# Optimization experiments

Measured on AMD Instinct MI355X. Metric: run time of the kernel, lower is better.

Reference implementation:

```python
import jax, jax.numpy as jnp
import numpy as np

N_NODES = 100000
N_EDGES = 600000
D_FEAT = 128
N_CLASSES = 40
K = 2


def setup_inputs() -> dict:
    key = jax.random.key(0)
    k1, k2, k3, k4, k5 = jax.random.split(key, 5)
    x = jax.random.normal(k1, (N_NODES, D_FEAT), dtype=jnp.float32)
    edge_index = jax.random.randint(k2, (2, N_EDGES), 0, N_NODES, dtype=jnp.int64)
    W = jax.random.normal(k3, (N_CLASSES, D_FEAT), dtype=jnp.float32) / np.sqrt(D_FEAT)
    b = jax.random.normal(k4, (N_CLASSES,), dtype=jnp.float32) * 0.01
    return {"x": x, "edge_index": edge_index, "W": W, "b": b}


def _gcn_norm(edge_index, num_nodes):
    # add self loops (PyG gcn_norm default), edge_weight = 1
    loop = jnp.arange(num_nodes, dtype=edge_index.dtype)
    src = jnp.concatenate([edge_index[0], loop])
    dst = jnp.concatenate([edge_index[1], loop])
    w = jnp.ones(src.shape[0], dtype=jnp.float32)
    deg = jax.ops.segment_sum(w, dst, num_segments=num_nodes)  # [N]
    dinv = jnp.where(deg > 0, 1.0 / jnp.sqrt(deg), 0.0)
    norm = dinv[src] * w * dinv[dst]  # D^-1/2 A_hat D^-1/2 edge weights
    return src, dst, norm


def reference(x, edge_index, W, b):
    # eval mode: dropout is identity
    src, dst, norm = _gcn_norm(edge_index, N_NODES)
    for _ in range(K):
        # message: x_j * norm, aggr='add' at target nodes
        x = jax.ops.segment_sum(x[src] * norm[:, None], dst, num_segments=N_NODES)
    logits = x @ W.T + b  # [N, C]
    return jax.nn.log_softmax(logits, axis=1)
```

## Files before the change

### kernel.cpp

```cpp
#include <hip/hip_runtime.h>

#define N_NODES   100000
#define N_EDGES   600000
#define D_FEAT    128
#define N_CLASSES 40
#define USTRIDE   64
#define MAXW      40

#define NPAD      100352
#define N_TILES   (N_NODES / 16)
#define G_GEMM    1568
#define EPB       384
#define G_ZERO    (NPAD / 4 / 256 + 1)

typedef __attribute__((ext_vector_type(8))) short bf16x8;
typedef __attribute__((ext_vector_type(4))) float f32x4;

__device__ __forceinline__ float bf2f(unsigned int h) { return __uint_as_float(h << 16); }
__device__ __forceinline__ unsigned int f2bf(float f) {
    unsigned int u = __float_as_uint(f);
    return (u + 0x7FFFu + ((u >> 16) & 1u)) >> 16;
}
__device__ __forceinline__ float4 up4(uint2 v) {
    return make_float4(bf2f(v.x & 0xFFFFu), bf2f(v.x >> 16),
                       bf2f(v.y & 0xFFFFu), bf2f(v.y >> 16));
}
__device__ __forceinline__ uint2 pk4(float4 f) {
    uint2 r;
    r.x = f2bf(f.x) | (f2bf(f.y) << 16);
    r.y = f2bf(f.z) | (f2bf(f.w) << 16);
    return r;
}


__global__ void k_zero_wconv(int4* __restrict__ deg4, const float* __restrict__ W,
                             uint4* __restrict__ wfrag) {
    int t = threadIdx.x;
    if (blockIdx.x < G_ZERO - 1) {
        int i = blockIdx.x * 256 + t;
        if (i < NPAD / 4) deg4[i] = make_int4(0, 0, 0, 0);
        return;
    }
    for (int idx = t; idx < 768; idx += 256) {
        int lane = idx & 63;
        int kc   = (idx >> 6) & 3;
        int ct   = idx >> 8;
        int r16  = lane & 15;
        int g    = lane >> 4;
        int j    = ct * 16 + r16;
        uint4 o = make_uint4(0u, 0u, 0u, 0u);
        if (j < N_CLASSES) {
            const float* wr = W + (size_t)j * D_FEAT + kc * 32 + g * 8;
            float4 w0 = *(const float4*)wr;
            float4 w1 = *(const float4*)(wr + 4);
            o.x = f2bf(w0.x) | (f2bf(w0.y) << 16);
            o.y = f2bf(w0.z) | (f2bf(w0.w) << 16);
            o.z = f2bf(w1.x) | (f2bf(w1.y) << 16);
            o.w = f2bf(w1.z) | (f2bf(w1.w) << 16);
        }
        wfrag[idx] = o;
    }
}


__global__ __launch_bounds__(256) void k_gemm_ell(const float* __restrict__ x,
                                                  const uint4* __restrict__ wfrag,
                                                  unsigned short* __restrict__ y0,
                                                  const int* __restrict__ esrc,
                                                  const int* __restrict__ edst,
                                                  int* __restrict__ deg,
                                                  int* __restrict__ ell) {
    int t = threadIdx.x;
    int wid = t >> 6;
    int lane = t & 63;
    int tile = (blockIdx.x & 7) + 8 * ((blockIdx.x >> 3) * 4 + wid);
    bool valid = tile < N_TILES;

    int r16 = lane & 15;
    int g   = lane >> 4;
    int node = tile * 16 + r16;

    int e0 = blockIdx.x * EPB + t;
    int e1 = e0 + 256;
    bool v0 = e0 < N_EDGES;
    bool v1 = (t < EPB - 256) && (e1 < N_EDGES);
    int d0 = 0, d1 = 0, src0 = 0, src1 = 0;
    if (v0) { d0 = edst[e0]; src0 = esrc[e0]; }
    if (v1) { d1 = edst[e1]; src1 = esrc[e1]; }

    uint4 wq[12];
    float4 xv[8];
    if (valid) {
#pragma unroll
        for (int f = 0; f < 12; ++f) wq[f] = wfrag[f * 64 + lane];
        const float4* xp = (const float4*)(x + (size_t)node * D_FEAT);
#pragma unroll
        for (int kc = 0; kc < 4; ++kc) {
            xv[kc * 2]     = xp[kc * 8 + g * 2];
            xv[kc * 2 + 1] = xp[kc * 8 + g * 2 + 1];
        }
    }

    int o0 = 0, o1 = 0;
    if (v0) o0 = atomicAdd(&deg[d0], 1);
    if (v1) o1 = atomicAdd(&deg[d1], 1);

    bf16x8 afrag[4];
    if (valid) {
#pragma unroll
        for (int kc = 0; kc < 4; ++kc) {
            union { bf16x8 v; unsigned int u[4]; } a;
            a.u[0] = f2bf(xv[kc * 2].x) | (f2bf(xv[kc * 2].y) << 16);
            a.u[1] = f2bf(xv[kc * 2].z) | (f2bf(xv[kc * 2].w) << 16);
            a.u[2] = f2bf(xv[kc * 2 + 1].x) | (f2bf(xv[kc * 2 + 1].y) << 16);
            a.u[3] = f2bf(xv[kc * 2 + 1].z) | (f2bf(xv[kc * 2 + 1].w) << 16);
            afrag[kc] = a.v;
        }
    }

    f32x4 z = {0.f, 0.f, 0.f, 0.f};
    f32x4 acc0 = z, acc1 = z, acc2 = z;
    if (valid) {
#pragma unroll
        for (int kc = 0; kc < 4; ++kc) {
            union { uint4 u4; bf16x8 v; } b0, b1, b2;
            b0.u4 = wq[kc];  b1.u4 = wq[4 + kc];  b2.u4 = wq[8 + kc];
            acc0 = __builtin_amdgcn_mfma_f32_16x16x32_bf16(b0.v, afrag[kc], acc0, 0, 0, 0);
            acc1 = __builtin_amdgcn_mfma_f32_16x16x32_bf16(b1.v, afrag[kc], acc1, 0, 0, 0);
            acc2 = __builtin_amdgcn_mfma_f32_16x16x32_bf16(b2.v, afrag[kc], acc2, 0, 0, 0);
        }
    }

    if (v0 && o0 < MAXW) ell[(size_t)o0 * N_NODES + d0] = src0;
    if (v1 && o1 < MAXW) ell[(size_t)o1 * N_NODES + d1] = src1;

    if (!valid) return;

    unsigned short* orow = y0 + (size_t)node * USTRIDE;
    uint2 s0, s1;
    s0.x = f2bf(acc0[0]) | (f2bf(acc0[1]) << 16);
    s0.y = f2bf(acc0[2]) | (f2bf(acc0[3]) << 16);
    *(uint2*)(orow + g * 4) = s0;
    s1.x = f2bf(acc1[0]) | (f2bf(acc1[1]) << 16);
    s1.y = f2bf(acc1[2]) | (f2bf(acc1[3]) << 16);
    *(uint2*)(orow + 16 + g * 4) = s1;
    if (g < 2) {
        uint2 s2;
        s2.x = f2bf(acc2[0]) | (f2bf(acc2[1]) << 16);
        s2.y = f2bf(acc2[2]) | (f2bf(acc2[3]) << 16);
        *(uint2*)(orow + 32 + g * 4) = s2;
    } else {
        *(uint4*)(orow + 32 + g * 8) = make_uint4(0u, 0u, 0u, 0u);
    }
    if (g == 1) *(uint4*)(orow + 40) = make_uint4(0u, 0u, 0u, 0u);
}


__global__ __launch_bounds__(256) void k_gather1(const unsigned short* __restrict__ y0,
                                                 unsigned short* __restrict__ u1,
                                                 const int* __restrict__ deg,
                                                 const int* __restrict__ ell) {
    int t = blockIdx.x * blockDim.x + threadIdx.x;
    int i = t >> 4;
    if (i >= N_NODES) return;
    int sub = t & 1;
    int par = (t >> 1) & 7;
    const uint2* yb = (const uint2*)y0;

    int degi = deg[i];
    float di = rsqrtf((float)(degi + 1));

    float4 a[5];
    if (par == 0) {
        const uint2* self = yb + (size_t)i * 16 + sub * 5;
#pragma unroll
        for (int r = 0; r < 5; ++r) {
            float4 v = up4(self[r]);
            a[r] = make_float4(v.x * di, v.y * di, v.z * di, v.w * di);
        }
    } else {
#pragma unroll
        for (int r = 0; r < 5; ++r) a[r] = make_float4(0.f, 0.f, 0.f, 0.f);
    }

    int nd = degi < MAXW ? degi : MAXW;
    for (int k = par; k < nd; k += 8) {
        int s = ell[(size_t)k * N_NODES + i];
        float ds = rsqrtf((float)(deg[s] + 1));
        const uint2* p = yb + (size_t)s * 16 + sub * 5;
        uint2 w[5];
#pragma unroll
        for (int r = 0; r < 5; ++r) w[r] = p[r];
#pragma unroll
        for (int r = 0; r < 5; ++r) {
            float4 v = up4(w[r]);
            a[r].x += v.x * ds; a[r].y += v.y * ds;
            a[r].z += v.z * ds; a[r].w += v.w * ds;
        }
    }

#pragma unroll
    for (int d = 2; d <= 8; d <<= 1) {
#pragma unroll
        for (int r = 0; r < 5; ++r) {
            a[r].x += __shfl_xor(a[r].x, d); a[r].y += __shfl_xor(a[r].y, d);
            a[r].z += __shfl_xor(a[r].z, d); a[r].w += __shfl_xor(a[r].w, d);
        }
    }

    unsigned short* orow = u1 + (size_t)i * USTRIDE;
    if (par == 0) {
        float s2 = di * di;
        uint2* o = (uint2*)orow + sub * 5;
#pragma unroll
        for (int r = 0; r < 5; ++r) {
            o[r] = pk4(make_float4(a[r].x * s2, a[r].y * s2, a[r].z * s2, a[r].w * s2));
        }
    } else if (par == 1) {
        *(uint4*)(orow + 40 + sub * 8) = make_uint4(0u, 0u, 0u, 0u);
    } else if (par == 2 && sub == 0) {
        *(uint4*)(orow + 56) = make_uint4(0u, 0u, 0u, 0u);
    }
}


__global__ __launch_bounds__(256) void k_gather_out(const unsigned short* __restrict__ u1,
                                                    float* __restrict__ out,
                                                    const int* __restrict__ deg,
                                                    const int* __restrict__ ell,
                                                    const float* __restrict__ bias) {
    int t = blockIdx.x * blockDim.x + threadIdx.x;
    int i = t >> 4;
    if (i >= N_NODES) return;
    int sub = t & 1;
    int par = (t >> 1) & 7;
    const uint2* yb = (const uint2*)u1;

    int degi = deg[i];
    float di = rsqrtf((float)(degi + 1));

    float4 a[5];
    if (par == 0) {
        const uint2* self = yb + (size_t)i * 16 + sub * 5;
#pragma unroll
        for (int r = 0; r < 5; ++r) a[r] = up4(self[r]);
    } else {
#pragma unroll
        for (int r = 0; r < 5; ++r) a[r] = make_float4(0.f, 0.f, 0.f, 0.f);
    }

    int nd = degi < MAXW ? degi : MAXW;
    for (int k = par; k < nd; k += 8) {
        int s = ell[(size_t)k * N_NODES + i];
        const uint2* p = yb + (size_t)s * 16 + sub * 5;
        uint2 w[5];
#pragma unroll
        for (int r = 0; r < 5; ++r) w[r] = p[r];
#pragma unroll
        for (int r = 0; r < 5; ++r) {
            float4 v = up4(w[r]);
            a[r].x += v.x; a[r].y += v.y; a[r].z += v.z; a[r].w += v.w;
        }
    }

#pragma unroll
    for (int d = 2; d <= 8; d <<= 1) {
#pragma unroll
        for (int r = 0; r < 5; ++r) {
            a[r].x += __shfl_xor(a[r].x, d); a[r].y += __shfl_xor(a[r].y, d);
            a[r].z += __shfl_xor(a[r].z, d); a[r].w += __shfl_xor(a[r].w, d);
        }
    }

    const float4* b4 = (const float4*)bias + sub * 5;
    float4 l[5];
    float m = -INFINITY;
#pragma unroll
    for (int r = 0; r < 5; ++r) {
        float4 b = b4[r];
        l[r].x = a[r].x * di + b.x;
        l[r].y = a[r].y * di + b.y;
        l[r].z = a[r].z * di + b.z;
        l[r].w = a[r].w * di + b.w;
        m = fmaxf(m, fmaxf(fmaxf(l[r].x, l[r].y), fmaxf(l[r].z, l[r].w)));
    }
    m = fmaxf(m, __shfl_xor(m, 1));
    float s = 0.f;
#pragma unroll
    for (int r = 0; r < 5; ++r) {
        s += __expf(l[r].x - m) + __expf(l[r].y - m)
           + __expf(l[r].z - m) + __expf(l[r].w - m);
    }
    s += __shfl_xor(s, 1);
    float lse = __logf(s) + m;

    if (par == 0) {
        float4* o = (float4*)out + (size_t)i * 10 + sub * 5;
#pragma unroll
        for (int r = 0; r < 5; ++r) {
            o[r] = make_float4(l[r].x - lse, l[r].y - lse, l[r].z - lse, l[r].w - lse);
        }
    }
}


extern "C" void kernel_launch(void* const* d_in, const int* in_sizes, int n_in,
                              void* d_out, int out_size, void* d_ws, size_t ws_size,
                              hipStream_t stream) {
    const float* x   = (const float*)d_in[0];
    const int*   ei  = (const int*)d_in[1];
    const float* W   = (const float*)d_in[2];
    const float* b   = (const float*)d_in[3];
    float*       out = (float*)d_out;

    const int* esrc = ei;
    const int* edst = ei + N_EDGES;

    int*   deg   = (int*)d_ws;
    uint4* wfrag = (uint4*)(deg + NPAD);
    int*   ell   = (int*)(deg + NPAD + 3072);
    unsigned short* y0 = (unsigned short*)(ell + (size_t)N_NODES * MAXW);
    unsigned short* u1 = y0 + (size_t)N_NODES * USTRIDE;

    const int B = 256;
    const int gG = (16 * N_NODES + B - 1) / B;

    k_zero_wconv<<<G_ZERO, B, 0, stream>>>((int4*)deg, W, wfrag);
    k_gemm_ell<<<G_GEMM, B, 0, stream>>>(x, wfrag, y0, esrc, edst, deg, ell);
    k_gather1  <<<gG, B, 0, stream>>>(y0, u1, deg, ell);
    k_gather_out<<<gG, B, 0, stream>>>(u1, out, deg, ell, b);
}
```

Before: 83.63 us.

## Split GEMM K-dimension across wave pairs with LDS reduction, doubling grid

```diff
diff --git a/kernel.cpp b/kernel.cpp
--- a/kernel.cpp
+++ b/kernel.cpp
@@ -9,8 +9,8 @@
 
 #define NPAD      100352
 #define N_TILES   (N_NODES / 16)
-#define G_GEMM    1568
-#define EPB       384
+#define G_GEMM    3128
+#define EPB       192
 #define G_ZERO    (NPAD / 4 / 256 + 1)
 
 typedef __attribute__((ext_vector_type(8))) short bf16x8;
@@ -71,50 +71,54 @@
                                                   int* __restrict__ deg,
                                                   int* __restrict__ ell) {
     int t = threadIdx.x;
-    int wid = t >> 6;
+    int wid  = t >> 6;
+    int pair = wid >> 1;
+    int h    = wid & 1;
     int lane = t & 63;
-    int tile = (blockIdx.x & 7) + 8 * ((blockIdx.x >> 3) * 4 + wid);
+    int tile = (blockIdx.x & 7) + 8 * ((blockIdx.x >> 3) * 2 + pair);
     bool valid = tile < N_TILES;
 
     int r16 = lane & 15;
     int g   = lane >> 4;
     int node = tile * 16 + r16;
 
+    __shared__ float lacc[12][128];
+
     int e0 = blockIdx.x * EPB + t;
-    int e1 = e0 + 256;
-    bool v0 = e0 < N_EDGES;
-    bool v1 = (t < EPB - 256) && (e1 < N_EDGES);
-    int d0 = 0, d1 = 0, src0 = 0, src1 = 0;
+    bool v0 = (t < EPB) && (e0 < N_EDGES);
+    int d0 = 0, src0 = 0;
     if (v0) { d0 = edst[e0]; src0 = esrc[e0]; }
-    if (v1) { d1 = edst[e1]; src1 = esrc[e1]; }
-
-    uint4 wq[12];
-    float4 xv[8];
+
+    uint4 wq[6];
+    float4 xv[4];
     if (valid) {
 #pragma unroll
-        for (int f = 0; f < 12; ++f) wq[f] = wfrag[f * 64 + lane];
+        for (int ct = 0; ct < 3; ++ct)
+#pragma unroll
+            for (int k2 = 0; k2 < 2; ++k2)
+                wq[ct * 2 + k2] = wfrag[(ct * 4 + 2 * h + k2) * 64 + lane];
         const float4* xp = (const float4*)(x + (size_t)node * D_FEAT);
 #pragma unroll
-        for (int kc = 0; kc < 4; ++kc) {
-            xv[kc * 2]     = xp[kc * 8 + g * 2];
-            xv[kc * 2 + 1] = xp[kc * 8 + g * 2 + 1];
-        }
-    }
-
-    int o0 = 0, o1 = 0;
+        for (int k2 = 0; k2 < 2; ++k2) {
+            int kc = 2 * h + k2;
+            xv[k2 * 2]     = xp[kc * 8 + g * 2];
+            xv[k2 * 2 + 1] = xp[kc * 8 + g * 2 + 1];
+        }
+    }
+
+    int o0 = 0;
     if (v0) o0 = atomicAdd(&deg[d0], 1);
-    if (v1) o1 = atomicAdd(&deg[d1], 1);
-
-    bf16x8 afrag[4];
+
+    bf16x8 afrag[2];
     if (valid) {
 #pragma unroll
-        for (int kc = 0; kc < 4; ++kc) {
+        for (int k2 = 0; k2 < 2; ++k2) {
             union { bf16x8 v; unsigned int u[4]; } a;
-            a.u[0] = f2bf(xv[kc * 2].x) | (f2bf(xv[kc * 2].y) << 16);
-            a.u[1] = f2bf(xv[kc * 2].z) | (f2bf(xv[kc * 2].w) << 16);
-            a.u[2] = f2bf(xv[kc * 2 + 1].x) | (f2bf(xv[kc * 2 + 1].y) << 16);
-            a.u[3] = f2bf(xv[kc * 2 + 1].z) | (f2bf(xv[kc * 2 + 1].w) << 16);
-            afrag[kc] = a.v;
+            a.u[0] = f2bf(xv[k2 * 2].x) | (f2bf(xv[k2 * 2].y) << 16);
+            a.u[1] = f2bf(xv[k2 * 2].z) | (f2bf(xv[k2 * 2].w) << 16);
+            a.u[2] = f2bf(xv[k2 * 2 + 1].x) | (f2bf(xv[k2 * 2 + 1].y) << 16);
+            a.u[3] = f2bf(xv[k2 * 2 + 1].z) | (f2bf(xv[k2 * 2 + 1].w) << 16);
+            afrag[k2] = a.v;
         }
     }
 
@@ -122,19 +126,34 @@
     f32x4 acc0 = z, acc1 = z, acc2 = z;
     if (valid) {
 #pragma unroll
-        for (int kc = 0; kc < 4; ++kc) {
+        for (int k2 = 0; k2 < 2; ++k2) {
             union { uint4 u4; bf16x8 v; } b0, b1, b2;
-            b0.u4 = wq[kc];  b1.u4 = wq[4 + kc];  b2.u4 = wq[8 + kc];
-            acc0 = __builtin_amdgcn_mfma_f32_16x16x32_bf16(b0.v, afrag[kc], acc0, 0, 0, 0);
-            acc1 = __builtin_amdgcn_mfma_f32_16x16x32_bf16(b1.v, afrag[kc], acc1, 0, 0, 0);
-            acc2 = __builtin_amdgcn_mfma_f32_16x16x32_bf16(b2.v, afrag[kc], acc2, 0, 0, 0);
+            b0.u4 = wq[k2];  b1.u4 = wq[2 + k2];  b2.u4 = wq[4 + k2];
+            acc0 = __builtin_amdgcn_mfma_f32_16x16x32_bf16(b0.v, afrag[k2], acc0, 0, 0, 0);
+            acc1 = __builtin_amdgcn_mfma_f32_16x16x32_bf16(b1.v, afrag[k2], acc1, 0, 0, 0);
+            acc2 = __builtin_amdgcn_mfma_f32_16x16x32_bf16(b2.v, afrag[k2], acc2, 0, 0, 0);
         }
     }
 
     if (v0 && o0 < MAXW) ell[(size_t)o0 * N_NODES + d0] = src0;
-    if (v1 && o1 < MAXW) ell[(size_t)o1 * N_NODES + d1] = src1;
-
-    if (!valid) return;
+
+    int li = pair * 64 + lane;
+    if (valid && h == 1) {
+#pragma unroll
+        for (int j = 0; j < 4; ++j) {
+            lacc[j][li]     = acc0[j];
+            lacc[4 + j][li] = acc1[j];
+            lacc[8 + j][li] = acc2[j];
+        }
+    }
+    __syncthreads();
+    if (!valid || h == 1) return;
+#pragma unroll
+    for (int j = 0; j < 4; ++j) {
+        acc0[j] += lacc[j][li];
+        acc1[j] += lacc[4 + j][li];
+        acc2[j] += lacc[8 + j][li];
+    }
 
     unsigned short* orow = y0 + (size_t)node * USTRIDE;
     uint2 s0, s1;
```

Result: no change. 83.27 us (-0.4%).
